# Kernel optimization log

Measured on AMD Instinct MI355X. Metric: run time of the kernel, lower is better.

The kernel has to match this reference:

```python
import jax, jax.numpy as jnp
import numpy as np

B, T = 256, 32
AIN, VIN, TIN = 128, 256, 768
H = 256                     # hidden size for all three LSTM subnets
TW0 = 4                     # layer-1 time window
NW = T // TW0               # 8 layer-1 windows == layer-2 time window
R = 16                      # rank
O0, O1 = 128, 64            # inter_node_out_dims
D1 = TW0 * 3 * H + 1        # 3073
D2 = NW * O0 + 1            # 1025
CONST_BIAS = 0.5
POLY_ORDER = 2              # per-layer (same for both layers here)
POLY_NORM = 1


def setup_inputs() -> dict:
    key = jax.random.key(0)
    ks = iter(jax.random.split(key, 32))
    def n(shape, std):
        return jax.random.normal(next(ks), shape, jnp.float32) * std
    def xav(fan_in, fan_out):
        return (2.0 / (fan_in + fan_out)) ** 0.5
    inp = {
        'audio_x': n((B, T, AIN), 1.0),
        'video_x': n((B, T, VIN), 1.0),
        'text_x':  n((B, T, TIN), 1.0),
        # LSTM params (PyTorch layout: W_ih (4H,in), W_hh (4H,H), gate order i,f,g,o)
        'aw_ih': n((4 * H, AIN), xav(AIN, H)), 'aw_hh': n((4 * H, H), xav(H, H)),
        'ab_ih': jnp.zeros((4 * H,), jnp.float32), 'ab_hh': jnp.zeros((4 * H,), jnp.float32),
        'vw_ih': n((4 * H, VIN), xav(VIN, H)), 'vw_hh': n((4 * H, H), xav(H, H)),
        'vb_ih': jnp.zeros((4 * H,), jnp.float32), 'vb_hh': jnp.zeros((4 * H,), jnp.float32),
        'txw_ih': n((4 * H, TIN), xav(TIN, H)), 'txw_hh': n((4 * H, H), xav(H, H)),
        'txb_ih': jnp.zeros((4 * H,), jnp.float32), 'txb_hh': jnp.zeros((4 * H,), jnp.float32),
        # stacked per-window PTP params (one ParameterList entry per window in torch)
        'l1_factor': n((NW, R, D1, O0), xav(D1, O0)),
        'l1_weight': n((NW, R), xav(1, R)),
        'l1_bias': jnp.zeros((NW, O0), jnp.float32),
        'l2_factor': n((1, R, D2, O1), xav(D2, O1)),
        'l2_weight': n((1, R), xav(1, R)),
        'l2_bias': jnp.zeros((1, O1), jnp.float32),
    }
    return inp


def _lstm(x, w_ih, w_hh, b_ih, b_hh):
    """Single-layer batch_first LSTM, zero init state (SubNet in eval: dropout off)."""
    Hh = w_hh.shape[1]
    xp = jnp.einsum('bti,gi->btg', x, w_ih) + b_ih + b_hh          # (B,T,4H)
    def step(carry, xt):
        h, c = carry
        g = xt + h @ w_hh.T
        i, f, gg, o = jnp.split(g, 4, axis=-1)
        i = jax.nn.sigmoid(i); f = jax.nn.sigmoid(f); o = jax.nn.sigmoid(o)
        gg = jnp.tanh(gg)
        c = f * c + i * gg
        h = o * jnp.tanh(c)
        return (h, c), h
    Bb = x.shape[0]
    init = (jnp.zeros((Bb, Hh), x.dtype), jnp.zeros((Bb, Hh), x.dtype))
    _, hs = jax.lax.scan(step, init, xp.transpose(1, 0, 2))         # (T,B,H)
    return hs.transpose(1, 0, 2)


def _ptp(nodes, tw, factor, weight, bias):
    """One ptp_layer with a single modal group; all time windows vectorized.
    nodes: (B,T,F) concat over modalities; factor (nW,R,D,O); weight (nW,R); bias (nW,O).
    """
    Bb, Tt, F = nodes.shape
    nw = Tt // tw
    x = nodes.reshape(Bb, nw, tw * F)
    const = jnp.full((Bb, nw, 1), CONST_BIAS, x.dtype)
    x = jnp.concatenate([const, x], axis=2)                         # (B,nW,D)
    z = jnp.einsum('bnd,nrdo->nbro', x, factor)                     # (nW,B,R,O)
    p = z
    for _ in range(POLY_ORDER):                                     # z^(order+1)
        p = p * z
    for _ in range(POLY_NORM):                                      # sign-sqrt norm
        p = jnp.sign(p) * jnp.sqrt(jnp.abs(p))
    p = p / jnp.linalg.norm(p, axis=-1, keepdims=True)              # euclid_norm
    out = jnp.einsum('nr,nbro->nbo', weight, p) + bias[:, None, :]  # (nW,B,O)
    return out.transpose(1, 0, 2)                                   # (B,nW,O)


def reference(audio_x, video_x, text_x,
              aw_ih, aw_hh, ab_ih, ab_hh,
              vw_ih, vw_hh, vb_ih, vb_hh,
              txw_ih, txw_hh, txb_ih, txb_hh,
              l1_factor, l1_weight, l1_bias,
              l2_factor, l2_weight, l2_bias):
    ah = _lstm(audio_x, aw_ih, aw_hh, ab_ih, ab_hh)
    vh = _lstm(video_x, vw_ih, vw_hh, vb_ih, vb_hh)
    th = _lstm(text_x, txw_ih, txw_hh, txb_ih, txb_hh)
    # modal_win==3: data_dict order is text('0'), audio('1'), video('2');
    # per-window torch.cat along feature dim == concat once over full time axis.
    cat1 = jnp.concatenate([th, ah, vh], axis=2)                    # (B,T,3H)
    f1 = _ptp(cat1, TW0, l1_factor, l1_weight, l1_bias)             # (B,NW,O0)
    f2 = _ptp(f1, NW, l2_factor, l2_weight, l2_bias)                # (B,1,O1)
    return f2.reshape(-1, O1)                                       # (B,O1)
```

## Files before the change

kernel.cpp:

```cpp
#include <hip/hip_runtime.h>
#include <hip/hip_bf16.h>


namespace {
constexpr int kB  = 256;
constexpr int kT  = 32;
constexpr int kH  = 256;
constexpr int k4H = 1024;
constexpr int kNW = 8;
constexpr int kR  = 16;
constexpr int kO0 = 128;
constexpr int kO1 = 64;
constexpr int kD1 = 3073;
constexpr int kD2 = 1025;
}

typedef __attribute__((ext_vector_type(8))) short short8;
typedef __attribute__((ext_vector_type(4))) float f32x4;
typedef __attribute__((ext_vector_type(4))) unsigned int u32x4;

typedef const __attribute__((address_space(1))) unsigned int* gas_u32p;
typedef __attribute__((address_space(3))) unsigned int* las_u32p;

__device__ __forceinline__ unsigned int pack2bf(float a, float b) {
    unsigned int ua = __builtin_bit_cast(unsigned int, a);
    unsigned int ub = __builtin_bit_cast(unsigned int, b);
    return (ua >> 16) | (ub & 0xffff0000u);
}
__device__ __forceinline__ float bflo(unsigned int u) {
    return __builtin_bit_cast(float, u << 16);
}
__device__ __forceinline__ float bfhi(unsigned int u) {
    return __builtin_bit_cast(float, u & 0xffff0000u);
}
__device__ __forceinline__ float sigm(float x) {
    return 1.f / (1.f + __expf(-x));
}
__device__ __forceinline__ float tanh_fast(float x) {
    float a = fabsf(x);
    float t = 1.f - 2.f / (__expf(2.f * a) + 1.f);
    return copysignf(t, x);
}
__device__ __forceinline__ uint2 gload2u(const unsigned short* p) {
    uint2 r;
    asm volatile("global_load_dwordx2 %0, %1, off" : "=v"(r) : "v"(p) : "memory");
    return r;
}

__global__ __launch_bounds__(512)
void k_mm_all(const float* __restrict__ A0, const float* __restrict__ A1,
              const float* __restrict__ A2,
              const float* __restrict__ W0, const float* __restrict__ W1,
              const float* __restrict__ W2,
              const float* __restrict__ bi0, const float* __restrict__ bi1,
              const float* __restrict__ bi2,
              const float* __restrict__ bh0, const float* __restrict__ bh1,
              const float* __restrict__ bh2,
              unsigned short* __restrict__ C0, unsigned short* __restrict__ C1,
              unsigned short* __restrict__ C2,
              const float* __restrict__ wa, const float* __restrict__ wv,
              const float* __restrict__ wtx, unsigned int* __restrict__ wfrag) {
    const int bx  = blockIdx.x;
    const int tid = threadIdx.x;

    if (bx >= 768) {
        int g = (bx - 768) * 512 + tid;
        int l  = g & 63;
        int gt = (g >> 6) & 3;
        int s  = (g >> 8) & 7;
        int w  = (g >> 11) & 15;
        int net = g >> 15;
        const float* W = (net == 0) ? wa : (net == 1) ? wv : wtx;
        const int col = gt * 256 + w * 16 + (l & 15);
        const int k0  = s * 32 + (l >> 4) * 8;
        const float* src = W + (size_t)col * 256 + k0;
        float4 f0 = *(const float4*)src;
        float4 f1 = *(const float4*)(src + 4);
        u32x4 v = { pack2bf(f0.x, f0.y), pack2bf(f0.z, f0.w),
                    pack2bf(f1.x, f1.y), pack2bf(f1.z, f1.w) };
        *(u32x4*)&wfrag[(size_t)g * 4] = v;
        return;
    }

    const int net = bx >> 8;
    const int mt  = (bx & 255) >> 3;
    const int nt  = bx & 7;
    const float* A  = (net == 0) ? A0 : (net == 1) ? A1 : A2;
    const float* W  = (net == 0) ? W0 : (net == 1) ? W1 : W2;
    const float* b1 = (net == 0) ? bi0 : (net == 1) ? bi1 : bi2;
    const float* b2 = (net == 0) ? bh0 : (net == 1) ? bh1 : bh2;
    unsigned short* C = (net == 0) ? C0 : (net == 1) ? C1 : C2;
    const int K = (net == 0) ? 128 : (net == 1) ? 256 : 768;

    __shared__ __align__(16) unsigned int As[256 * 20];
    __shared__ __align__(16) unsigned int Bs[128 * 20];
    const int lane = tid & 63;
    const int wid  = tid >> 6;
    const int wm   = wid >> 1, wn = wid & 1;
    const int m0 = mt * 256, n0 = nt * 128;
    const int nstep = K >> 5;

    const int ar = tid >> 1, akq = (tid & 1) * 16;
    const int br = tid >> 2, bkq = (tid & 3) * 8;
    const float* ap = A + (size_t)(m0 + ar) * K + akq;
    const int nn = n0 + br;
    const int worow = (nn & 3) * 256 + (nn >> 6) * 16 + ((nn >> 2) & 15);
    const float* wp = W + (size_t)worow * K + bkq;

    float4 aR[4], bR[2];
    auto loadA = [&](int s) {
#pragma unroll
        for (int i = 0; i < 4; ++i) aR[i] = *(const float4*)(ap + s * 32 + i * 4);
    };
    auto loadB = [&](int s) {
#pragma unroll
        for (int i = 0; i < 2; ++i) bR[i] = *(const float4*)(wp + s * 32 + i * 4);
    };

    f32x4 acc[4][4];
#pragma unroll
    for (int i = 0; i < 4; ++i)
#pragma unroll
        for (int j = 0; j < 4; ++j) acc[i][j] = (f32x4){0.f, 0.f, 0.f, 0.f};

    loadA(0); loadB(0);
    for (int s = 0; s < nstep; ++s) {
        __syncthreads();
        {
            u32x4 w0 = { pack2bf(aR[0].x, aR[0].y), pack2bf(aR[0].z, aR[0].w),
                         pack2bf(aR[1].x, aR[1].y), pack2bf(aR[1].z, aR[1].w) };
            u32x4 w1 = { pack2bf(aR[2].x, aR[2].y), pack2bf(aR[2].z, aR[2].w),
                         pack2bf(aR[3].x, aR[3].y), pack2bf(aR[3].z, aR[3].w) };
            *(u32x4*)&As[ar * 20 + (akq >> 1)]     = w0;
            *(u32x4*)&As[ar * 20 + (akq >> 1) + 4] = w1;
            u32x4 v0 = { pack2bf(bR[0].x, bR[0].y), pack2bf(bR[0].z, bR[0].w),
                         pack2bf(bR[1].x, bR[1].y), pack2bf(bR[1].z, bR[1].w) };
            *(u32x4*)&Bs[br * 20 + (bkq >> 1)] = v0;
        }
        __syncthreads();
        if (s + 1 < nstep) { loadA(s + 1); loadB(s + 1); }
        short8 af[4], bf[4];
#pragma unroll
        for (int i = 0; i < 4; ++i)
            af[i] = __builtin_bit_cast(short8,
                *(const u32x4*)&As[(wm * 64 + i * 16 + (lane & 15)) * 20 + (lane >> 4) * 4]);
#pragma unroll
        for (int j = 0; j < 4; ++j)
            bf[j] = __builtin_bit_cast(short8,
                *(const u32x4*)&Bs[(wn * 64 + j * 16 + (lane & 15)) * 20 + (lane >> 4) * 4]);
#pragma unroll
        for (int i = 0; i < 4; ++i)
#pragma unroll
            for (int j = 0; j < 4; ++j)
                acc[i][j] = __builtin_amdgcn_mfma_f32_16x16x32_bf16(af[i], bf[j], acc[i][j], 0, 0, 0);
    }
#pragma unroll
    for (int i = 0; i < 4; ++i) {
#pragma unroll
        for (int j = 0; j < 4; ++j) {
            const int col  = n0 + wn * 64 + j * 16 + (lane & 15);
            const int ocol = (col & 3) * 256 + (col >> 6) * 16 + ((col >> 2) & 15);
            const float badd = b1[ocol] + b2[ocol];
#pragma unroll
            for (int e = 0; e < 4; ++e) {
                const int row = m0 + wm * 64 + i * 16 + (lane >> 4) * 4 + e;
                const float v = acc[i][j][e] + badd;
                C[(size_t)row * 1024 + col] =
                    (unsigned short)(__builtin_bit_cast(unsigned int, v) >> 16);
            }
        }
    }
}

__global__ __launch_bounds__(1024, 4)
void k_lstm6(const unsigned short* __restrict__ xp_a, const unsigned short* __restrict__ xp_v,
             const unsigned short* __restrict__ xp_t, const unsigned int* __restrict__ wfrag,
             unsigned short* __restrict__ hp) {
    const int bg  = blockIdx.x;
    const int net = blockIdx.y;
    const int tid = threadIdx.x;
    const int l   = tid & 63;
    const int w   = tid >> 6;
    const unsigned short* xp = (net == 0) ? xp_a : (net == 1) ? xp_v : xp_t;
    const int coloff = (net == 0) ? 256 : (net == 1) ? 512 : 0;

    __shared__ __align__(16) unsigned short hA[8192];
    __shared__ __align__(16) unsigned int Wring[32768];

    for (int i = tid; i < 4096; i += 1024) ((unsigned int*)hA)[i] = 0u;

    const int q  = l & 15;
    const int r0 = (l >> 4) * 4;
    const int d  = w * 16 + q;

    const char* wbase = (const char*)wfrag + (size_t)(net * 16 + w) * 32768 + l * 16;
    unsigned int* wslot = &Wring[w * 2048];

    const unsigned short* xr0 = xp + ((size_t)(bg * 16 + r0) * 32) * 1024 + w * 64 + q * 4;

    const unsigned int rbase = (unsigned int)q * 512;
    const unsigned int rxor  = (unsigned int)(q & 7) << 4;
    const unsigned int kofs  = (unsigned int)(l >> 4) * 16;

    float cc[4] = {0.f, 0.f, 0.f, 0.f};

    auto issue_slab = [&](int slab, int slot) {
#pragma unroll
        for (int g = 0; g < 4; ++g) {
            const void* gp = (const void*)(wbase + slab * 4096 + g * 1024);
            void* lp = (void*)(wslot + slot * 1024 + g * 256);
            __builtin_amdgcn_global_load_lds(
                (gas_u32p)(size_t)gp,
                (las_u32p)(unsigned int)(size_t)lp, 16, 0, 0);
        }
    };

    issue_slab(0, 0);
    issue_slab(1, 1);
    asm volatile("s_waitcnt lgkmcnt(0)" ::: "memory");
    __builtin_amdgcn_s_barrier();

    for (int t = 0; t < kT; ++t) {
        const unsigned short* xr = xr0 + (size_t)t * 1024;
        uint2 xq0 = gload2u(xr);
        uint2 xq1 = gload2u(xr + 32768);
        uint2 xq2 = gload2u(xr + 65536);
        uint2 xq3 = gload2u(xr + 98304);

        const unsigned int rbuf = (unsigned int)(t & 1) * 8192;
        const unsigned int wbuf = 8192u - rbuf;

        f32x4 acc[4];
#pragma unroll
        for (int g = 0; g < 4; ++g) acc[g] = (f32x4){0.f, 0.f, 0.f, 0.f};

#pragma unroll
        for (int s = 0; s < 8; ++s) {
            if (s < 2) asm volatile("s_waitcnt vmcnt(8)" ::: "memory");
            else       asm volatile("s_waitcnt vmcnt(4)" ::: "memory");
            __builtin_amdgcn_sched_barrier(0);
            u32x4 af = *(const u32x4*)((const char*)hA + rbuf + rbase
                                       + (((unsigned)(s * 64) + kofs) ^ rxor));
            const unsigned int* wp = wslot + (s & 1) * 1024;
            u32x4 b0 = *(const u32x4*)(wp + 0 * 256 + l * 4);
            u32x4 b1 = *(const u32x4*)(wp + 1 * 256 + l * 4);
            u32x4 b2 = *(const u32x4*)(wp + 2 * 256 + l * 4);
            u32x4 b3 = *(const u32x4*)(wp + 3 * 256 + l * 4);
            acc[0] = __builtin_amdgcn_mfma_f32_16x16x32_bf16(
                __builtin_bit_cast(short8, af), __builtin_bit_cast(short8, b0), acc[0], 0, 0, 0);
            acc[1] = __builtin_amdgcn_mfma_f32_16x16x32_bf16(
                __builtin_bit_cast(short8, af), __builtin_bit_cast(short8, b1), acc[1], 0, 0, 0);
            acc[2] = __builtin_amdgcn_mfma_f32_16x16x32_bf16(
                __builtin_bit_cast(short8, af), __builtin_bit_cast(short8, b2), acc[2], 0, 0, 0);
            acc[3] = __builtin_amdgcn_mfma_f32_16x16x32_bf16(
                __builtin_bit_cast(short8, af), __builtin_bit_cast(short8, b3), acc[3], 0, 0, 0);
            __builtin_amdgcn_sched_barrier(0);
            issue_slab((s + 2) & 7, s & 1);
        }

        asm volatile("s_waitcnt vmcnt(8)" ::: "memory");
        __builtin_amdgcn_sched_barrier(0);

        float hv[4];
        {
            float gi, gf, gg, go;
            gi = acc[0][0] + bflo(xq0.x); gf = acc[1][0] + bfhi(xq0.x);
            gg = acc[2][0] + bflo(xq0.y); go = acc[3][0] + bfhi(xq0.y);
            cc[0] = sigm(gf) * cc[0] + sigm(gi) * tanh_fast(gg); hv[0] = sigm(go) * tanh_fast(cc[0]);
            gi = acc[0][1] + bflo(xq1.x); gf = acc[1][1] + bfhi(xq1.x);
            gg = acc[2][1] + bflo(xq1.y); go = acc[3][1] + bfhi(xq1.y);
            cc[1] = sigm(gf) * cc[1] + sigm(gi) * tanh_fast(gg); hv[1] = sigm(go) * tanh_fast(cc[1]);
            gi = acc[0][2] + bflo(xq2.x); gf = acc[1][2] + bfhi(xq2.x);
            gg = acc[2][2] + bflo(xq2.y); go = acc[3][2] + bfhi(xq2.y);
            cc[2] = sigm(gf) * cc[2] + sigm(gi) * tanh_fast(gg); hv[2] = sigm(go) * tanh_fast(cc[2]);
            gi = acc[0][3] + bflo(xq3.x); gf = acc[1][3] + bfhi(xq3.x);
            gg = acc[2][3] + bflo(xq3.y); go = acc[3][3] + bfhi(xq3.y);
            cc[3] = sigm(gf) * cc[3] + sigm(gi) * tanh_fast(gg); hv[3] = sigm(go) * tanh_fast(cc[3]);
        }

        const int kk = (t & 3) * 768 + coloff + d;
        const int sp2 = kk >> 5;
        unsigned short* hpb = hp +
            ((((size_t)((t >> 2) * 96 + sp2) * 16 + bg) * 64
              + (unsigned)(r0 | (((kk >> 3) & 3) << 4))) * 8 + (kk & 7));
#pragma unroll
        for (int e = 0; e < 4; ++e) {
            const unsigned short hb =
                (unsigned short)(__builtin_bit_cast(unsigned int, hv[e]) >> 16);
            const int row = r0 + e;
            *(unsigned short*)((char*)hA + wbuf + (unsigned)row * 512
                               + (((unsigned)(2 * d)) ^ (((unsigned)(row & 7)) << 4))) = hb;
            hpb[e * 8] = hb;
        }
        asm volatile("s_waitcnt lgkmcnt(0)" ::: "memory");
        __builtin_amdgcn_s_barrier();
    }
}

__global__ __launch_bounds__(512)
void k_ptp1_mfma(const unsigned int* __restrict__ hp, const float* __restrict__ factor,
                 float* __restrict__ z1) {
    __shared__ __align__(16) unsigned char Bs[128 * 80];
    const int tid  = threadIdx.x;
    const int lane = tid & 63;
    const int wid  = tid >> 6;
    const int r = blockIdx.x;
    const int n = blockIdx.y;

    const int bo = tid & 127;
    const int bc = tid >> 7;
    const float* fp = factor + ((size_t)(n * kR + r) * kD1 + 1 + bc * 8) * kO0 + bo;
    const unsigned int* ha = hp + (size_t)n * 96 * 4096 + lane * 4;

    f32x4 acc[2][8];
#pragma unroll
    for (int i = 0; i < 2; ++i)
#pragma unroll
        for (int j = 0; j < 8; ++j) acc[i][j] = (f32x4){0.f, 0.f, 0.f, 0.f};

    u32x4 pkb[2];
    u32x4 af[2][2];
    auto loadB = [&](int s, int qq) {
        float rv[8];
#pragma unroll
        for (int e = 0; e < 8; ++e)
            rv[e] = fp[((size_t)s * 32 + e) * kO0];
        pkb[qq] = (u32x4){ pack2bf(rv[0], rv[1]), pack2bf(rv[2], rv[3]),
                           pack2bf(rv[4], rv[5]), pack2bf(rv[6], rv[7]) };
    };
    auto loadA = [&](int s, int qq) {
#pragma unroll
        for (int i = 0; i < 2; ++i)
            af[qq][i] = *(const u32x4*)(ha + ((size_t)s * 16 + (wid * 2 + i)) * 256);
    };
    loadB(0, 0); loadA(0, 0);
#pragma unroll 2
    for (int s = 0; s < 96; ++s) {
        const int qq = s & 1;
        __syncthreads();
        *(u32x4*)(Bs + bo * 80 + bc * 16) = pkb[qq];
        __syncthreads();
        if (s + 1 < 96) { loadB(s + 1, qq ^ 1); loadA(s + 1, qq ^ 1); }
        short8 bf[8];
#pragma unroll
        for (int j = 0; j < 8; ++j)
            bf[j] = __builtin_bit_cast(short8,
                *(const u32x4*)(Bs + (j * 16 + (lane & 15)) * 80 + (lane >> 4) * 16));
#pragma unroll
        for (int i = 0; i < 2; ++i)
#pragma unroll
            for (int j = 0; j < 8; ++j)
                acc[i][j] = __builtin_amdgcn_mfma_f32_16x16x32_bf16(
                    __builtin_bit_cast(short8, af[qq][i]), bf[j], acc[i][j], 0, 0, 0);
    }
    const size_t zb = (size_t)n * 256;
#pragma unroll
    for (int i = 0; i < 2; ++i) {
#pragma unroll
        for (int j = 0; j < 8; ++j) {
            const int col = j * 16 + (lane & 15);
#pragma unroll
            for (int e = 0; e < 4; ++e) {
                const int row = (wid * 2 + i) * 16 + (lane >> 4) * 4 + e;
                z1[((zb + row) * kR + r) * kO0 + col] = acc[i][j][e];
            }
        }
    }
}

__global__ __launch_bounds__(64)
void k_ptp1_post(const float* __restrict__ z1, const float* __restrict__ factor,
                 const float* __restrict__ w, const float* __restrict__ bias,
                 float* __restrict__ f1) {
    const int b = blockIdx.x;
    const int n = blockIdx.y;
    const int o = threadIdx.x;
    float sv0[kR], sv1[kR], nrm[kR];
    const size_t zbase = ((size_t)n * kB + b) * kR * kO0;
#pragma unroll
    for (int r = 0; r < kR; ++r) {
        const size_t zo = zbase + r * kO0 + o;
        const size_t fo = (size_t)(n * kR + r) * kD1 * kO0 + o;
        float v0 = z1[zo] + 0.5f * factor[fo];
        float v1 = z1[zo + 64] + 0.5f * factor[fo + 64];
        float a0 = fabsf(v0), a1 = fabsf(v1);
        float s0 = copysignf(a0 * sqrtf(a0), v0);
        float s1 = copysignf(a1 * sqrtf(a1), v1);
        sv0[r] = s0; sv1[r] = s1;
        float t = s0 * s0 + s1 * s1;
#pragma unroll
        for (int off = 1; off < 64; off <<= 1) t += __shfl_xor(t, off, 64);
        nrm[r] = sqrtf(t);
    }
    float out0 = bias[n * kO0 + o];
    float out1 = bias[n * kO0 + o + 64];
#pragma unroll
    for (int r = 0; r < kR; ++r) {
        const float wr = w[n * kR + r];
        out0 += wr * sv0[r] / nrm[r];
        out1 += wr * sv1[r] / nrm[r];
    }
    f1[((size_t)b * kNW + n) * kO0 + o] = out0;
    f1[((size_t)b * kNW + n) * kO0 + o + 64] = out1;
}

__global__ __launch_bounds__(256)
void k_ptp2_gemm(const float* __restrict__ f1flat, const float* __restrict__ factor2,
                 float* __restrict__ z2) {
    const int b0 = blockIdx.x * 32;
    const int r  = blockIdx.y;
    const int tx = threadIdx.x & 63;
    const int ty = threadIdx.x >> 6;
    __shared__ float xs[32][128];
    __shared__ float Fs[128][64];
    float acc[8];
#pragma unroll
    for (int i = 0; i < 8; ++i) acc[i] = 0.f;
    const float* F = factor2 + (size_t)r * kD2 * kO1;

    for (int k0 = 0; k0 < kD2; k0 += 128) {
        const int len = min(128, kD2 - k0);
        {
            const int row = threadIdx.x >> 3;
            const int c0  = (threadIdx.x & 7) * 16;
#pragma unroll
            for (int i = 0; i < 16; ++i) {
                int k = k0 + c0 + i;
                float v = (k == 0) ? 0.5f
                        : (k < kD2 ? f1flat[(size_t)(b0 + row) * 1024 + (k - 1)] : 0.f);
                xs[row][c0 + i] = v;
            }
        }
        {
#pragma unroll
            for (int i = 0; i < 8; ++i) {
                const int u  = threadIdx.x + i * 256;
                const int dd = u >> 4;
                const int oc = (u & 15) * 4;
                float4 v = (k0 + dd < kD2)
                    ? *(const float4*)(F + (size_t)(k0 + dd) * kO1 + oc)
                    : make_float4(0.f, 0.f, 0.f, 0.f);
                *(float4*)&Fs[dd][oc] = v;
            }
        }
        __syncthreads();
        for (int dd = 0; dd < len; ++dd) {
            float wv = Fs[dd][tx];
#pragma unroll
            for (int i = 0; i < 8; ++i) acc[i] = fmaf(xs[ty * 8 + i][dd], wv, acc[i]);
        }
        __syncthreads();
    }
#pragma unroll
    for (int i = 0; i < 8; ++i) {
        const int b = b0 + ty * 8 + i;
        z2[((size_t)b * kR + r) * kO1 + tx] = acc[i];
    }
}

__global__ __launch_bounds__(64)
void k_ptp2_post(const float* __restrict__ z2, const float* __restrict__ w2,
                 const float* __restrict__ b2, float* __restrict__ out) {
    const int b = blockIdx.x;
    const int o = threadIdx.x;
    float sv[kR], nrm[kR];
#pragma unroll
    for (int r = 0; r < kR; ++r) {
        float v = z2[((size_t)b * kR + r) * kO1 + o];
        float a = fabsf(v);
        float s = copysignf(a * sqrtf(a), v);
        sv[r] = s;
        float t = s * s;
#pragma unroll
        for (int off = 1; off < 64; off <<= 1) t += __shfl_xor(t, off, 64);
        nrm[r] = sqrtf(t);
    }
    float acc = b2[o];
#pragma unroll
    for (int r = 0; r < kR; ++r) acc += w2[r] * sv[r] / nrm[r];
    out[(size_t)b * kO1 + o] = acc;
}

extern "C" void kernel_launch(void* const* d_in, const int* in_sizes, int n_in,
                              void* d_out, int out_size, void* d_ws, size_t ws_size,
                              hipStream_t stream) {
    const float* audio_x  = (const float*)d_in[0];
    const float* video_x  = (const float*)d_in[1];
    const float* text_x   = (const float*)d_in[2];
    const float* aw_ih    = (const float*)d_in[3];
    const float* aw_hh    = (const float*)d_in[4];
    const float* ab_ih    = (const float*)d_in[5];
    const float* ab_hh    = (const float*)d_in[6];
    const float* vw_ih    = (const float*)d_in[7];
    const float* vw_hh    = (const float*)d_in[8];
    const float* vb_ih    = (const float*)d_in[9];
    const float* vb_hh    = (const float*)d_in[10];
    const float* txw_ih   = (const float*)d_in[11];
    const float* txw_hh   = (const float*)d_in[12];
    const float* txb_ih   = (const float*)d_in[13];
    const float* txb_hh   = (const float*)d_in[14];
    const float* l1_factor = (const float*)d_in[15];
    const float* l1_weight = (const float*)d_in[16];
    const float* l1_bias   = (const float*)d_in[17];
    const float* l2_factor = (const float*)d_in[18];
    const float* l2_weight = (const float*)d_in[19];
    const float* l2_bias   = (const float*)d_in[20];

    float* ws = (float*)d_ws;
    unsigned short* xp_a = (unsigned short*)ws;
    unsigned short* xp_v = (unsigned short*)(ws + 4194304);
    unsigned short* xp_t = (unsigned short*)(ws + 8388608);
    unsigned short* hp   = (unsigned short*)(ws + 12582912);
    unsigned int* wfrag  = (unsigned int*)(ws + 15728640);
    float* z1 = ws;
    float* f1 = ws + 8388608;
    float* z2 = ws + 8388608 + 262144;

    k_mm_all<<<960, 512, 0, stream>>>(audio_x, video_x, text_x,
                                      aw_ih, vw_ih, txw_ih,
                                      ab_ih, vb_ih, txb_ih,
                                      ab_hh, vb_hh, txb_hh,
                                      xp_a, xp_v, xp_t,
                                      aw_hh, vw_hh, txw_hh, wfrag);

    k_lstm6<<<dim3(16, 3), 1024, 0, stream>>>(xp_a, xp_v, xp_t, wfrag, hp);

    k_ptp1_mfma<<<dim3(16, 8), 512, 0, stream>>>((const unsigned int*)hp, l1_factor, z1);
    k_ptp1_post<<<dim3(256, 8), 64, 0, stream>>>(z1, l1_factor, l1_weight, l1_bias, f1);

    k_ptp2_gemm<<<dim3(8, 16), 256, 0, stream>>>(f1, l2_factor, z2);
    k_ptp2_post<<<256, 64, 0, stream>>>(z2, l2_weight, l2_bias, (float*)d_out);
}
```

Before: 461.1 us.

## Hold LSTM recurrent weights in registers with 8 waves and split PTP1 over batch

The LSTM recurrence kernel moves from 16 waves that each handle 16 hidden units to 8 waves that each handle 32. Recurrent weight slabs are streamed from global memory straight into VGPRs with dwordx4 loads instead of going through an LDS ring via global_load_lds. The input projections for the next step are prefetched after the current step. The weight fragment layout and the xp column permutation in the input GEMM are changed to match, and the PTP1 MFMA kernel gains a z-dimension of 2 to split rows, doubling its block count. In exchange the LSTM kernel carries much higher register pressure and runs half as many waves to hide latency.

Result: slower. 549.3 us (+19.1%).

```diff
diff --git a/kernel.cpp b/kernel.cpp
--- a/kernel.cpp
+++ b/kernel.cpp
@@ -19,9 +19,6 @@
 typedef __attribute__((ext_vector_type(4))) float f32x4;
 typedef __attribute__((ext_vector_type(4))) unsigned int u32x4;
 
-typedef const __attribute__((address_space(1))) unsigned int* gas_u32p;
-typedef __attribute__((address_space(3))) unsigned int* las_u32p;
-
 __device__ __forceinline__ unsigned int pack2bf(float a, float b) {
     unsigned int ua = __builtin_bit_cast(unsigned int, a);
     unsigned int ub = __builtin_bit_cast(unsigned int, b);
@@ -41,10 +38,8 @@
     float t = 1.f - 2.f / (__expf(2.f * a) + 1.f);
     return copysignf(t, x);
 }
-__device__ __forceinline__ uint2 gload2u(const unsigned short* p) {
-    uint2 r;
-    asm volatile("global_load_dwordx2 %0, %1, off" : "=v"(r) : "v"(p) : "memory");
-    return r;
+__device__ __forceinline__ void gload4u(u32x4& dst, const void* p) {
+    asm volatile("global_load_dwordx4 %0, %1, off" : "=v"(dst) : "v"(p) : "memory");
 }
 
 __global__ __launch_bounds__(512)
@@ -65,13 +60,13 @@
 
     if (bx >= 768) {
         int g = (bx - 768) * 512 + tid;
-        int l  = g & 63;
-        int gt = (g >> 6) & 3;
-        int s  = (g >> 8) & 7;
-        int w  = (g >> 11) & 15;
+        int l   = g & 63;
+        int ct  = (g >> 6) & 7;
+        int s   = (g >> 9) & 7;
+        int w   = (g >> 12) & 7;
         int net = g >> 15;
         const float* W = (net == 0) ? wa : (net == 1) ? wv : wtx;
-        const int col = gt * 256 + w * 16 + (l & 15);
+        const int col = (ct & 3) * 256 + w * 32 + (ct >> 2) * 16 + (l & 15);
         const int k0  = s * 32 + (l >> 4) * 8;
         const float* src = W + (size_t)col * 256 + k0;
         float4 f0 = *(const float4*)src;
@@ -104,7 +99,8 @@
     const int br = tid >> 2, bkq = (tid & 3) * 8;
     const float* ap = A + (size_t)(m0 + ar) * K + akq;
     const int nn = n0 + br;
-    const int worow = (nn & 3) * 256 + (nn >> 6) * 16 + ((nn >> 2) & 15);
+    const int wct = nn & 7;
+    const int worow = (wct & 3) * 256 + (nn >> 7) * 32 + (wct >> 2) * 16 + ((nn >> 3) & 15);
     const float* wp = W + (size_t)worow * K + bkq;
 
     float4 aR[4], bR[2];
@@ -158,8 +154,9 @@
     for (int i = 0; i < 4; ++i) {
 #pragma unroll
         for (int j = 0; j < 4; ++j) {
-            const int col  = n0 + wn * 64 + j * 16 + (lane & 15);
-            const int ocol = (col & 3) * 256 + (col >> 6) * 16 + ((col >> 2) & 15);
+            const int col = n0 + wn * 64 + j * 16 + (lane & 15);
+            const int cct = col & 7;
+            const int ocol = (cct & 3) * 256 + (col >> 7) * 32 + (cct >> 2) * 16 + ((col >> 3) & 15);
             const float badd = b1[ocol] + b2[ocol];
 #pragma unroll
             for (int e = 0; e < 4; ++e) {
@@ -172,8 +169,8 @@
     }
 }
 
-__global__ __launch_bounds__(1024, 4)
-void k_lstm6(const unsigned short* __restrict__ xp_a, const unsigned short* __restrict__ xp_v,
+__global__ __launch_bounds__(512, 2)
+void k_lstm8(const unsigned short* __restrict__ xp_a, const unsigned short* __restrict__ xp_v,
              const unsigned short* __restrict__ xp_t, const unsigned int* __restrict__ wfrag,
              unsigned short* __restrict__ hp) {
     const int bg  = blockIdx.x;
@@ -185,113 +182,107 @@
     const int coloff = (net == 0) ? 256 : (net == 1) ? 512 : 0;
 
     __shared__ __align__(16) unsigned short hA[8192];
-    __shared__ __align__(16) unsigned int Wring[32768];
-
-    for (int i = tid; i < 4096; i += 1024) ((unsigned int*)hA)[i] = 0u;
+    for (int i = tid; i < 4096; i += 512) ((unsigned int*)hA)[i] = 0u;
 
     const int q  = l & 15;
     const int r0 = (l >> 4) * 4;
-    const int d  = w * 16 + q;
-
-    const char* wbase = (const char*)wfrag + (size_t)(net * 16 + w) * 32768 + l * 16;
-    unsigned int* wslot = &Wring[w * 2048];
-
-    const unsigned short* xr0 = xp + ((size_t)(bg * 16 + r0) * 32) * 1024 + w * 64 + q * 4;
+    const int d0 = w * 32 + q;
+
+    const unsigned int* wb = wfrag + (size_t)(net * 8 + w) * 16384 + l * 4;
+    const unsigned short* xr0 = xp + ((size_t)(bg * 16 + r0) * 32) * 1024 + w * 128 + q * 8;
 
     const unsigned int rbase = (unsigned int)q * 512;
     const unsigned int rxor  = (unsigned int)(q & 7) << 4;
     const unsigned int kofs  = (unsigned int)(l >> 4) * 16;
 
-    float cc[4] = {0.f, 0.f, 0.f, 0.f};
-
-    auto issue_slab = [&](int slab, int slot) {
-#pragma unroll
-        for (int g = 0; g < 4; ++g) {
-            const void* gp = (const void*)(wbase + slab * 4096 + g * 1024);
-            void* lp = (void*)(wslot + slot * 1024 + g * 256);
-            __builtin_amdgcn_global_load_lds(
-                (gas_u32p)(size_t)gp,
-                (las_u32p)(unsigned int)(size_t)lp, 16, 0, 0);
-        }
-    };
-
-    issue_slab(0, 0);
-    issue_slab(1, 1);
+    float cc0[4] = {0.f, 0.f, 0.f, 0.f};
+    float cc1[4] = {0.f, 0.f, 0.f, 0.f};
+    u32x4 b[2][8];
+    u32x4 xq[4];
+
+#pragma unroll
+    for (int s = 0; s < 2; ++s)
+#pragma unroll
+        for (int ct = 0; ct < 8; ++ct)
+            gload4u(b[s][ct], wb + (s * 8 + ct) * 256);
+#pragma unroll
+    for (int e = 0; e < 4; ++e)
+        gload4u(xq[e], xr0 + (size_t)e * 32768);
+
     asm volatile("s_waitcnt lgkmcnt(0)" ::: "memory");
     __builtin_amdgcn_s_barrier();
 
+#pragma unroll 1
     for (int t = 0; t < kT; ++t) {
-        const unsigned short* xr = xr0 + (size_t)t * 1024;
-        uint2 xq0 = gload2u(xr);
-        uint2 xq1 = gload2u(xr + 32768);
-        uint2 xq2 = gload2u(xr + 65536);
-        uint2 xq3 = gload2u(xr + 98304);
-
         const unsigned int rbuf = (unsigned int)(t & 1) * 8192;
         const unsigned int wbuf = 8192u - rbuf;
 
-        f32x4 acc[4];
-#pragma unroll
-        for (int g = 0; g < 4; ++g) acc[g] = (f32x4){0.f, 0.f, 0.f, 0.f};
+        f32x4 acc[8];
+#pragma unroll
+        for (int ct = 0; ct < 8; ++ct) acc[ct] = (f32x4){0.f, 0.f, 0.f, 0.f};
 
 #pragma unroll
         for (int s = 0; s < 8; ++s) {
-            if (s < 2) asm volatile("s_waitcnt vmcnt(8)" ::: "memory");
-            else       asm volatile("s_waitcnt vmcnt(4)" ::: "memory");
+            if (s < 2) asm volatile("s_waitcnt vmcnt(12)" ::: "memory");
+            else       asm volatile("s_waitcnt vmcnt(8)" ::: "memory");
             __builtin_amdgcn_sched_barrier(0);
             u32x4 af = *(const u32x4*)((const char*)hA + rbuf + rbase
                                        + (((unsigned)(s * 64) + kofs) ^ rxor));
-            const unsigned int* wp = wslot + (s & 1) * 1024;
-            u32x4 b0 = *(const u32x4*)(wp + 0 * 256 + l * 4);
-            u32x4 b1 = *(const u32x4*)(wp + 1 * 256 + l * 4);
-            u32x4 b2 = *(const u32x4*)(wp + 2 * 256 + l * 4);
-            u32x4 b3 = *(const u32x4*)(wp + 3 * 256 + l * 4);
-            acc[0] = __builtin_amdgcn_mfma_f32_16x16x32_bf16(
-                __builtin_bit_cast(short8, af), __builtin_bit_cast(short8, b0), acc[0], 0, 0, 0);
-            acc[1] = __builtin_amdgcn_mfma_f32_16x16x32_bf16(
-                __builtin_bit_cast(short8, af), __builtin_bit_cast(short8, b1), acc[1], 0, 0, 0);
-            acc[2] = __builtin_amdgcn_mfma_f32_16x16x32_bf16(
-                __builtin_bit_cast(short8, af), __builtin_bit_cast(short8, b2), acc[2], 0, 0, 0);
-            acc[3] = __builtin_amdgcn_mfma_f32_16x16x32_bf16(
-                __builtin_bit_cast(short8, af), __builtin_bit_cast(short8, b3), acc[3], 0, 0, 0);
+#pragma unroll
+            for (int ct = 0; ct < 8; ++ct)
+                acc[ct] = __builtin_amdgcn_mfma_f32_16x16x32_bf16(
+                    __builtin_bit_cast(short8, af),
+                    __builtin_bit_cast(short8, b[s & 1][ct]), acc[ct], 0, 0, 0);
             __builtin_amdgcn_sched_barrier(0);
-            issue_slab((s + 2) & 7, s & 1);
-        }
-
-        asm volatile("s_waitcnt vmcnt(8)" ::: "memory");
-        __builtin_amdgcn_sched_barrier(0);
-
-        float hv[4];
-        {
-            float gi, gf, gg, go;
-            gi = acc[0][0] + bflo(xq0.x); gf = acc[1][0] + bfhi(xq0.x);
-            gg = acc[2][0] + bflo(xq0.y); go = acc[3][0] + bfhi(xq0.y);
-            cc[0] = sigm(gf) * cc[0] + sigm(gi) * tanh_fast(gg); hv[0] = sigm(go) * tanh_fast(cc[0]);
-            gi = acc[0][1] + bflo(xq1.x); gf = acc[1][1] + bfhi(xq1.x);
-            gg = acc[2][1] + bflo(xq1.y); go = acc[3][1] + bfhi(xq1.y);
-            cc[1] = sigm(gf) * cc[1] + sigm(gi) * tanh_fast(gg); hv[1] = sigm(go) * tanh_fast(cc[1]);
-            gi = acc[0][2] + bflo(xq2.x); gf = acc[1][2] + bfhi(xq2.x);
-            gg = acc[2][2] + bflo(xq2.y); go = acc[3][2] + bfhi(xq2.y);
-            cc[2] = sigm(gf) * cc[2] + sigm(gi) * tanh_fast(gg); hv[2] = sigm(go) * tanh_fast(cc[2]);
-            gi = acc[0][3] + bflo(xq3.x); gf = acc[1][3] + bfhi(xq3.x);
-            gg = acc[2][3] + bflo(xq3.y); go = acc[3][3] + bfhi(xq3.y);
-            cc[3] = sigm(gf) * cc[3] + sigm(gi) * tanh_fast(gg); hv[3] = sigm(go) * tanh_fast(cc[3]);
-        }
-
-        const int kk = (t & 3) * 768 + coloff + d;
-        const int sp2 = kk >> 5;
+            const int ns = (s + 2) & 7;
+#pragma unroll
+            for (int ct = 0; ct < 8; ++ct)
+                gload4u(b[s & 1][ct], wb + (ns * 8 + ct) * 256);
+        }
+
+        float hv0[4], hv1[4];
+#pragma unroll
+        for (int e = 0; e < 4; ++e) {
+            float gi = acc[0][e] + bflo(xq[e][0]);
+            float gf = acc[1][e] + bfhi(xq[e][0]);
+            float gg = acc[2][e] + bflo(xq[e][1]);
+            float go = acc[3][e] + bfhi(xq[e][1]);
+            cc0[e] = sigm(gf) * cc0[e] + sigm(gi) * tanh_fast(gg);
+            hv0[e] = sigm(go) * tanh_fast(cc0[e]);
+            gi = acc[4][e] + bflo(xq[e][2]);
+            gf = acc[5][e] + bfhi(xq[e][2]);
+            gg = acc[6][e] + bflo(xq[e][3]);
+            go = acc[7][e] + bfhi(xq[e][3]);
+            cc1[e] = sigm(gf) * cc1[e] + sigm(gi) * tanh_fast(gg);
+            hv1[e] = sigm(go) * tanh_fast(cc1[e]);
+        }
+
+        const int kk0 = (t & 3) * 768 + coloff + d0;
+        const int sp  = kk0 >> 5;
         unsigned short* hpb = hp +
-            ((((size_t)((t >> 2) * 96 + sp2) * 16 + bg) * 64
-              + (unsigned)(r0 | (((kk >> 3) & 3) << 4))) * 8 + (kk & 7));
+            ((((size_t)((t >> 2) * 96 + sp) * 16 + bg) * 64
+              + (unsigned)(r0 | ((q >> 3) << 4))) * 8 + (kk0 & 7));
 #pragma unroll
         for (int e = 0; e < 4; ++e) {
-            const unsigned short hb =
-                (unsigned short)(__builtin_bit_cast(unsigned int, hv[e]) >> 16);
+            const unsigned short h0 =
+                (unsigned short)(__builtin_bit_cast(unsigned int, hv0[e]) >> 16);
+            const unsigned short h1 =
+                (unsigned short)(__builtin_bit_cast(unsigned int, hv1[e]) >> 16);
             const int row = r0 + e;
+            const unsigned int sxor = ((unsigned)(row & 7)) << 4;
             *(unsigned short*)((char*)hA + wbuf + (unsigned)row * 512
-                               + (((unsigned)(2 * d)) ^ (((unsigned)(row & 7)) << 4))) = hb;
-            hpb[e * 8] = hb;
-        }
+                               + (((unsigned)(2 * d0)) ^ sxor)) = h0;
+            *(unsigned short*)((char*)hA + wbuf + (unsigned)row * 512
+                               + (((unsigned)(2 * d0 + 32)) ^ sxor)) = h1;
+            hpb[e * 8] = h0;
+            hpb[256 + e * 8] = h1;
+        }
+
+        const int tn = (t < kT - 1) ? (t + 1) : (kT - 1);
+#pragma unroll
+        for (int e = 0; e < 4; ++e)
+            gload4u(xq[e], xr0 + (size_t)tn * 1024 + (size_t)e * 32768);
+
         asm volatile("s_waitcnt lgkmcnt(0)" ::: "memory");
         __builtin_amdgcn_s_barrier();
     }
@@ -304,22 +295,21 @@
     const int tid  = threadIdx.x;
     const int lane = tid & 63;
     const int wid  = tid >> 6;
-    const int r = blockIdx.x;
-    const int n = blockIdx.y;
+    const int r  = blockIdx.x;
+    const int n  = blockIdx.y;
+    const int bz = blockIdx.z;
 
     const int bo = tid & 127;
     const int bc = tid >> 7;
     const float* fp = factor + ((size_t)(n * kR + r) * kD1 + 1 + bc * 8) * kO0 + bo;
     const unsigned int* ha = hp + (size_t)n * 96 * 4096 + lane * 4;
 
-    f32x4 acc[2][8];
-#pragma unroll
-    for (int i = 0; i < 2; ++i)
-#pragma unroll
-        for (int j = 0; j < 8; ++j) acc[i][j] = (f32x4){0.f, 0.f, 0.f, 0.f};
+    f32x4 acc[8];
+#pragma unroll
+    for (int j = 0; j < 8; ++j) acc[j] = (f32x4){0.f, 0.f, 0.f, 0.f};
 
     u32x4 pkb[2];
-    u32x4 af[2][2];
+    u32x4 af[2];
     auto loadB = [&](int s, int qq) {
         float rv[8];
 #pragma unroll
@@ -329,9 +319,7 @@
                            pack2bf(rv[4], rv[5]), pack2bf(rv[6], rv[7]) };
     };
     auto loadA = [&](int s, int qq) {
-#pragma unroll
-        for (int i = 0; i < 2; ++i)
-            af[qq][i] = *(const u32x4*)(ha + ((size_t)s * 16 + (wid * 2 + i)) * 256);
+        af[qq] = *(const u32x4*)(ha + ((size_t)s * 16 + bz * 8 + wid) * 256);
     };
     loadB(0, 0); loadA(0, 0);
 #pragma unroll 2
@@ -347,23 +335,18 @@
             bf[j] = __builtin_bit_cast(short8,
                 *(const u32x4*)(Bs + (j * 16 + (lane & 15)) * 80 + (lane >> 4) * 16));
 #pragma unroll
-        for (int i = 0; i < 2; ++i)
-#pragma unroll
-            for (int j = 0; j < 8; ++j)
-                acc[i][j] = __builtin_amdgcn_mfma_f32_16x16x32_bf16(
-                    __builtin_bit_cast(short8, af[qq][i]), bf[j], acc[i][j], 0, 0, 0);
+        for (int j = 0; j < 8; ++j)
+            acc[j] = __builtin_amdgcn_mfma_f32_16x16x32_bf16(
+                __builtin_bit_cast(short8, af[qq]), bf[j], acc[j], 0, 0, 0);
     }
     const size_t zb = (size_t)n * 256;
 #pragma unroll
-    for (int i = 0; i < 2; ++i) {
-#pragma unroll
-        for (int j = 0; j < 8; ++j) {
-            const int col = j * 16 + (lane & 15);
-#pragma unroll
-            for (int e = 0; e < 4; ++e) {
-                const int row = (wid * 2 + i) * 16 + (lane >> 4) * 4 + e;
-                z1[((zb + row) * kR + r) * kO0 + col] = acc[i][j][e];
-            }
+    for (int j = 0; j < 8; ++j) {
+        const int col = j * 16 + (lane & 15);
+#pragma unroll
+        for (int e = 0; e < 4; ++e) {
+            const int row = (bz * 8 + wid) * 16 + (lane >> 4) * 4 + e;
+            z1[((zb + row) * kR + r) * kO0 + col] = acc[j][e];
         }
     }
 }
@@ -523,9 +506,9 @@
                                       xp_a, xp_v, xp_t,
                                       aw_hh, vw_hh, txw_hh, wfrag);
 
-    k_lstm6<<<dim3(16, 3), 1024, 0, stream>>>(xp_a, xp_v, xp_t, wfrag, hp);
-
-    k_ptp1_mfma<<<dim3(16, 8), 512, 0, stream>>>((const unsigned int*)hp, l1_factor, z1);
+    k_lstm8<<<dim3(16, 3), 512, 0, stream>>>(xp_a, xp_v, xp_t, wfrag, hp);
+
+    k_ptp1_mfma<<<dim3(16, 8, 2), 512, 0, stream>>>((const unsigned int*)hp, l1_factor, z1);
     k_ptp1_post<<<dim3(256, 8), 64, 0, stream>>>(z1, l1_factor, l1_weight, l1_bias, f1);
 
     k_ptp2_gemm<<<dim3(8, 16), 256, 0, stream>>>(f1, l2_factor, z2);
```
